# Optimization experiments

Measured on AMD Instinct MI355X. Metric: run time of the kernel, lower is better.

Reference implementation:

```python
import jax, jax.numpy as jnp
import numpy as np

NUM_ITERATIONS = 3
NUM_ROUTES = 6912  # 32*6*6*6


def _squash(t):
    # t: [..., O]; squash along last dim
    sq = jnp.sum(t * t, axis=-1, keepdims=True)
    return sq * t / ((1.0 + sq) * jnp.sqrt(sq))


def setup_inputs() -> dict:
    key = jax.random.key(0)
    k1, k2 = jax.random.split(key)
    B, R, I, C, O = 64, NUM_ROUTES, 8, 10, 16
    x = jax.random.normal(k1, (B, R, I), dtype=jnp.float32)
    route_weights = jax.random.normal(k2, (C, R, I, O), dtype=jnp.float32)
    return {"x": x, "route_weights": route_weights}


def reference(x, route_weights):
    # x: [B, R, I]; route_weights: [C, R, I, O]
    # priors = x[None,:,:,None,:] @ W[:,None,:,:,:] -> [C, B, R, 1, O]
    priors = jnp.einsum('bri,crio->cbro', x, route_weights)[:, :, :, None, :]
    logits = jnp.zeros_like(priors)  # [C, B, R, 1, O]
    outputs = None
    for i in range(NUM_ITERATIONS):
        # softmax over routes (dim=2), matching custom softmax(input, dim=2)
        probs = jax.nn.softmax(logits, axis=2)
        outputs = _squash(jnp.sum(probs * priors, axis=2, keepdims=True))  # [C,B,1,1,O]
        if i != NUM_ROUTES - 1:  # always true in original (num_routes >> iters)
            delta = jnp.sum(priors * outputs, axis=-1, keepdims=True)  # [C,B,R,1,1]
            logits = logits + delta
    return outputs
```

## Files before the change

kernel.cpp:

```cpp
#include <hip/hip_runtime.h>
#include <math.h>

#define BB 64
#define RR 6912
#define II 8
#define CC 10
#define OO 16
#define RPB 64
#define NCH 108
#define NGRP 8
#define MRG_PAD 20
#define LDSF (4*64*MRG_PAD + 4*64)

typedef _Float16 h2 __attribute__((ext_vector_type(2)));
typedef _Float16 half8 __attribute__((ext_vector_type(8)));
typedef float f32x16 __attribute__((ext_vector_type(16)));
union HV { int4 v; h2 h[4]; half8 h8; };

__global__ __launch_bounds__(256) void prep_kernel(
    const float* __restrict__ x, int4* __restrict__ xth4,
    const float4* __restrict__ w4, int4* __restrict__ wh4)
{
    __shared__ __align__(16) float4 lds4[64 * 34];
    const int t = threadIdx.x;
    const int bid = blockIdx.x;

    if (bid < 432) {
        const int rblk = bid >> 2;
        const int bblk = bid & 3;
        const int r0 = rblk * 64, b0 = bblk * 16;
        {
            const int rl = t & 63;
            const int bl0 = t >> 6;
#pragma unroll
            for (int kb = 0; kb < 4; ++kb) {
                const int bl = kb * 4 + bl0;
                const float4* src = (const float4*)(x + ((size_t)(b0 + bl) * RR + (r0 + rl)) * II);
                lds4[rl * 34 + bl * 2 + 0] = src[0];
                lds4[rl * 34 + bl * 2 + 1] = src[1];
            }
        }
        __syncthreads();
        {
            const int bl = t & 15;
            const int rw0 = t >> 4;
#pragma unroll
            for (int kr = 0; kr < 4; ++kr) {
                const int rw = kr * 16 + rw0;
                float4 a = lds4[rw * 34 + bl * 2 + 0];
                float4 bq = lds4[rw * 34 + bl * 2 + 1];
                HV u;
                u.h[0] = h2{(_Float16)a.x,  (_Float16)a.y};
                u.h[1] = h2{(_Float16)a.z,  (_Float16)a.w};
                u.h[2] = h2{(_Float16)bq.x, (_Float16)bq.y};
                u.h[3] = h2{(_Float16)bq.z, (_Float16)bq.w};
                xth4[(size_t)(r0 + rw) * BB + (b0 + bl)] = u.v;
            }
        }
    } else {
        _Float16* wl = (_Float16*)lds4;
        const int wblk = bid - 432;
        const int rp = t >> 5;
        const int i  = (t >> 2) & 7;
        const int o0 = (t & 3) * 4;
#pragma unroll 1
        for (int sb = 0; sb < 8; ++sb) {
            const int blk8 = wblk * 8 + sb;
            const float4 v = w4[(size_t)blk8 * 256 + t];
            _Float16* wb = wl + (sb & 1) * 1024;
            wb[(rp * 16 + o0 + 0) * 8 + i] = (_Float16)v.x;
            wb[(rp * 16 + o0 + 1) * 8 + i] = (_Float16)v.y;
            wb[(rp * 16 + o0 + 2) * 8 + i] = (_Float16)v.z;
            wb[(rp * 16 + o0 + 3) * 8 + i] = (_Float16)v.w;
            __syncthreads();
            if (t < 128) wh4[(size_t)blk8 * 128 + t] = ((const int4*)wb)[t];
        }
    }
}

template <int MODE>
__global__ __launch_bounds__(256, 4) void pass_kernel(
    const int4* __restrict__ xth4, const int4* __restrict__ wh4,
    const float* __restrict__ ov_in,
    float* __restrict__ pacc, float* __restrict__ pz)
{
    __shared__ __align__(16) float lds[LDSF];
    int4* wlds = (int4*)lds;

    const int bid = blockIdx.x;
    const int w = (bid & 7) * 135 + (bid >> 3);
    const int chunk = w / 10;
    const int c = w - chunk * 10;

    const int t = threadIdx.x;
    const int wv = t >> 6;
    const int l = t & 63;
    const int b = l & 31;
    const int hi = l >> 5;
    const int aquad = (l >> 4) & 1;
    const bool aact = (aquad == hi);

    {
        const int4* src = wh4 + (size_t)(c * (RR / 8) + chunk * 8) * 128;
#pragma unroll
        for (int k = 0; k < 4; ++k) wlds[k * 256 + t] = src[k * 256 + t];
    }

    float accA[8], accB[8];
#pragma unroll
    for (int j = 0; j < 8; ++j) { accA[j] = 0.f; accB[j] = 0.f; }
    float ZA = 0.f, ZB = 0.f;

    float ovA[8], ovB[8];
    if (MODE != 0) {
        const float* pa = ov_in + ((size_t)c * BB + b) * OO + 4 * hi;
        const float* pb = ov_in + ((size_t)c * BB + 32 + b) * OO + 4 * hi;
        float4 a0 = *(const float4*)(pa);
        float4 a1 = *(const float4*)(pa + 8);
        float4 b0 = *(const float4*)(pb);
        float4 b1 = *(const float4*)(pb + 8);
        ovA[0]=a0.x; ovA[1]=a0.y; ovA[2]=a0.z; ovA[3]=a0.w;
        ovA[4]=a1.x; ovA[5]=a1.y; ovA[6]=a1.z; ovA[7]=a1.w;
        ovB[0]=b0.x; ovB[1]=b0.y; ovB[2]=b0.z; ovB[3]=b0.w;
        ovB[4]=b1.x; ovB[5]=b1.y; ovB[6]=b1.z; ovB[7]=b1.w;
    }

    __syncthreads();

    const int rbase = chunk * RPB + wv * 16;

    f32x16 cA, cB, zf;
#pragma unroll
    for (int q = 0; q < 16; ++q) { cA[q] = 0.f; cB[q] = 0.f; zf[q] = 0.f; }

    HV xc0, xc1, xn0, xn1;
    xc0.v = xth4[(size_t)(rbase + hi) * BB + b];
    xc1.v = xth4[(size_t)(rbase + hi) * BB + 32 + b];
    xn0 = xc0; xn1 = xc1;

#pragma unroll 1
    for (int g = 0; g < NGRP; ++g) {
        if (g + 1 < NGRP) {
            const int rn = rbase + (g + 1) * 2 + hi;
            xn0.v = xth4[(size_t)rn * BB + b];
            xn1.v = xth4[(size_t)rn * BB + 32 + b];
        }
        const int rl0 = wv * 16 + g * 2;
        HV wq;
        wq.v = wlds[(rl0 + aquad) * 16 + (l & 15)];
        if (!aact) wq.v = make_int4(0, 0, 0, 0);

        if (MODE == 0) {
            cA = __builtin_amdgcn_mfma_f32_32x32x16_f16(wq.h8, xc0.h8, cA, 0, 0, 0);
            cB = __builtin_amdgcn_mfma_f32_32x32x16_f16(wq.h8, xc1.h8, cB, 0, 0, 0);
        } else {
            f32x16 p0 = __builtin_amdgcn_mfma_f32_32x32x16_f16(wq.h8, xc0.h8, zf, 0, 0, 0);
            f32x16 p1 = __builtin_amdgcn_mfma_f32_32x32x16_f16(wq.h8, xc1.h8, zf, 0, 0, 0);

            float dA0 = 0.f, dA1 = 0.f, dB0 = 0.f, dB1 = 0.f;
#pragma unroll
            for (int j = 0; j < 8; ++j) {
                dA0 = fmaf(p0[j],     ovA[j], dA0);
                dA1 = fmaf(p0[j + 8], ovA[j], dA1);
                dB0 = fmaf(p1[j],     ovB[j], dB0);
                dB1 = fmaf(p1[j + 8], ovB[j], dB1);
            }
            dA0 += __shfl_xor(dA0, 32);
            dA1 += __shfl_xor(dA1, 32);
            dB0 += __shfl_xor(dB0, 32);
            dB1 += __shfl_xor(dB1, 32);
            const float eA0 = __expf(dA0), eA1 = __expf(dA1);
            const float eB0 = __expf(dB0), eB1 = __expf(dB1);
            ZA += eA0 + eA1; ZB += eB0 + eB1;
#pragma unroll
            for (int j = 0; j < 8; ++j) {
                accA[j] = fmaf(eA0, p0[j], fmaf(eA1, p0[j + 8], accA[j]));
                accB[j] = fmaf(eB0, p1[j], fmaf(eB1, p1[j + 8], accB[j]));
            }
        }
        xc0 = xn0; xc1 = xn1;
    }

    if (MODE == 0) {
#pragma unroll
        for (int j = 0; j < 8; ++j) {
            accA[j] = cA[j] + cA[j + 8];
            accB[j] = cB[j] + cB[j + 8];
        }
    }

    __syncthreads();

    {
        float* m0 = lds + (wv * 64 + b) * MRG_PAD + 4 * hi;
        *(float4*)(m0)     = make_float4(accA[0], accA[1], accA[2], accA[3]);
        *(float4*)(m0 + 8) = make_float4(accA[4], accA[5], accA[6], accA[7]);
        float* m1 = lds + (wv * 64 + 32 + b) * MRG_PAD + 4 * hi;
        *(float4*)(m1)     = make_float4(accB[0], accB[1], accB[2], accB[3]);
        *(float4*)(m1 + 8) = make_float4(accB[4], accB[5], accB[6], accB[7]);
        if (MODE != 0 && hi == 0) {
            float* zr = lds + 4 * 64 * MRG_PAD;
            zr[wv * 64 + b] = ZA;
            zr[wv * 64 + 32 + b] = ZB;
        }
    }
    __syncthreads();

    {
        const int b2 = t >> 2, q = t & 3;
        float4 sum = make_float4(0.f, 0.f, 0.f, 0.f);
#pragma unroll
        for (int w2 = 0; w2 < 4; ++w2) {
            const float4 v = *(const float4*)(lds + (w2 * 64 + b2) * MRG_PAD + q * 4);
            sum.x += v.x; sum.y += v.y; sum.z += v.z; sum.w += v.w;
        }
        *(float4*)(pacc + (((size_t)(c * NCH + chunk) * BB + b2) * OO) + q * 4) = sum;
        if (MODE != 0 && q == 0) {
            const float* zr = lds + 4 * 64 * MRG_PAD;
            float z = 0.f;
#pragma unroll
            for (int w2 = 0; w2 < 4; ++w2) z += zr[w2 * 64 + b2];
            pz[(size_t)(c * NCH + chunk) * BB + b2] = z;
        }
    }
}

template <int MODE>
__global__ __launch_bounds__(256) void combine_kernel(
    const float* __restrict__ pacc, const float* __restrict__ pz,
    const float* __restrict__ out0, float* __restrict__ outw)
{
    __shared__ float lsum[256];
    __shared__ float lz[16];
    const int cb = blockIdx.x;
    const int c = cb >> 6, b = cb & 63;
    const int t = threadIdx.x;
    const int o = t & 15, g = t >> 4;

    float s = 0.f, zl = 0.f;
    for (int p = g; p < NCH; p += 16) {
        s += pacc[((size_t)(c * NCH + p) * BB + b) * OO + o];
        if (MODE != 0 && o == 0) zl += pz[(size_t)(c * NCH + p) * BB + b];
    }
    lsum[t] = s;
    if (MODE != 0 && o == 0) lz[g] = zl;
    __syncthreads();

    if (g == 0) {
#pragma unroll
        for (int k = 1; k < 16; ++k) s += lsum[k * 16 + o];
        if (MODE != 0) {
            float Zt = 0.f;
#pragma unroll
            for (int k = 0; k < 16; ++k) Zt += lz[k];
            s /= Zt;
        } else {
            s *= (1.0f / RR);
        }
        float sq = s * s;
#pragma unroll
        for (int w = 1; w < 16; w <<= 1) sq += __shfl_xor(sq, w);
        float val = s * sqrtf(sq) / (1.f + sq);
        if (MODE == 1) val += out0[(size_t)cb * OO + o];
        outw[(size_t)cb * OO + o] = val;
    }
}

extern "C" void kernel_launch(void* const* d_in, const int* in_sizes, int n_in,
                              void* d_out, int out_size, void* d_ws, size_t ws_size,
                              hipStream_t stream)
{
    const float* x = (const float*)d_in[0];
    const float* w = (const float*)d_in[1];
    float* out = (float*)d_out;

    float* ws = (float*)d_ws;
    float* xth    = ws;
    float* wh     = xth + (size_t)RR * BB * 4;
    float* pacc   = wh + (size_t)CC * RR * 64;
    float* pz     = pacc + (size_t)CC * NCH * BB * OO;
    float* out0   = pz + (size_t)CC * NCH * BB;
    float* outsum = out0 + CC * BB * OO;

    int4* xth4 = (int4*)xth;
    int4* wh4  = (int4*)wh;
    const float4* w4 = (const float4*)w;

    prep_kernel<<<dim3(432 + 1080), dim3(256), 0, stream>>>(x, xth4, w4, wh4);

    const dim3 gp(CC * NCH), bp(256);
    const dim3 gc(CC * BB), bc(256);

    pass_kernel<0><<<gp, bp, 0, stream>>>(xth4, wh4, nullptr, pacc, pz);
    combine_kernel<0><<<gc, bc, 0, stream>>>(pacc, pz, nullptr, out0);
    pass_kernel<1><<<gp, bp, 0, stream>>>(xth4, wh4, out0, pacc, pz);
    combine_kernel<1><<<gc, bc, 0, stream>>>(pacc, pz, out0, outsum);
    pass_kernel<2><<<gp, bp, 0, stream>>>(xth4, wh4, outsum, pacc, pz);
    combine_kernel<2><<<gc, bc, 0, stream>>>(pacc, pz, nullptr, out);
}
```

Baseline: 136.1 us.

## Simplify weight conversion and deepen x prefetch in pass kernel

The weight-prep path drops the LDS-staged transpose loop in favour of one thread per (route, o) that gathers 8 strided floats and writes one packed fp16 int4. The grid grows so each block handles 16 routes instead of 64. Separately, the pass kernel's x operand prefetch becomes a 4-deep register ring with the group loop fully unrolled, which hides more global-load latency. The costs are more uncoalesced strided reads in prep and higher register pressure in the pass kernel.

```diff
diff --git a/kernel.cpp b/kernel.cpp
--- a/kernel.cpp
+++ b/kernel.cpp
@@ -19,7 +19,7 @@
 
 __global__ __launch_bounds__(256) void prep_kernel(
     const float* __restrict__ x, int4* __restrict__ xth4,
-    const float4* __restrict__ w4, int4* __restrict__ wh4)
+    const float* __restrict__ w, int4* __restrict__ wh4)
 {
     __shared__ __align__(16) float4 lds4[64 * 34];
     const int t = threadIdx.x;
@@ -58,23 +58,19 @@
             }
         }
     } else {
-        _Float16* wl = (_Float16*)lds4;
         const int wblk = bid - 432;
-        const int rp = t >> 5;
-        const int i  = (t >> 2) & 7;
-        const int o0 = (t & 3) * 4;
-#pragma unroll 1
-        for (int sb = 0; sb < 8; ++sb) {
-            const int blk8 = wblk * 8 + sb;
-            const float4 v = w4[(size_t)blk8 * 256 + t];
-            _Float16* wb = wl + (sb & 1) * 1024;
-            wb[(rp * 16 + o0 + 0) * 8 + i] = (_Float16)v.x;
-            wb[(rp * 16 + o0 + 1) * 8 + i] = (_Float16)v.y;
-            wb[(rp * 16 + o0 + 2) * 8 + i] = (_Float16)v.z;
-            wb[(rp * 16 + o0 + 3) * 8 + i] = (_Float16)v.w;
-            __syncthreads();
-            if (t < 128) wh4[(size_t)blk8 * 128 + t] = ((const int4*)wb)[t];
-        }
+        const int rl = t >> 4;
+        const int o  = t & 15;
+        const size_t base = (size_t)wblk * 16 + rl;
+        const float* src = w + base * 128 + o;
+        float v0 = src[0 * 16], v1 = src[1 * 16], v2 = src[2 * 16], v3 = src[3 * 16];
+        float v4 = src[4 * 16], v5 = src[5 * 16], v6 = src[6 * 16], v7 = src[7 * 16];
+        HV u;
+        u.h[0] = h2{(_Float16)v0, (_Float16)v1};
+        u.h[1] = h2{(_Float16)v2, (_Float16)v3};
+        u.h[2] = h2{(_Float16)v4, (_Float16)v5};
+        u.h[3] = h2{(_Float16)v6, (_Float16)v7};
+        wh4[base * 16 + o] = u.v;
     }
 }
 
@@ -133,17 +129,21 @@
 #pragma unroll
     for (int q = 0; q < 16; ++q) { cA[q] = 0.f; cB[q] = 0.f; zf[q] = 0.f; }
 
-    HV xc0, xc1, xn0, xn1;
-    xc0.v = xth4[(size_t)(rbase + hi) * BB + b];
-    xc1.v = xth4[(size_t)(rbase + hi) * BB + 32 + b];
-    xn0 = xc0; xn1 = xc1;
-
-#pragma unroll 1
+    HV xq0[4], xq1[4];
+#pragma unroll
+    for (int g = 0; g < 4; ++g) {
+        const int rn = rbase + g * 2 + hi;
+        xq0[g].v = xth4[(size_t)rn * BB + b];
+        xq1[g].v = xth4[(size_t)rn * BB + 32 + b];
+    }
+
+#pragma unroll
     for (int g = 0; g < NGRP; ++g) {
-        if (g + 1 < NGRP) {
-            const int rn = rbase + (g + 1) * 2 + hi;
-            xn0.v = xth4[(size_t)rn * BB + b];
-            xn1.v = xth4[(size_t)rn * BB + 32 + b];
+        HV xc0 = xq0[g & 3], xc1 = xq1[g & 3];
+        if (g + 4 < NGRP) {
+            const int rn = rbase + (g + 4) * 2 + hi;
+            xq0[g & 3].v = xth4[(size_t)rn * BB + b];
+            xq1[g & 3].v = xth4[(size_t)rn * BB + 32 + b];
         }
         const int rl0 = wv * 16 + g * 2;
         HV wq;
@@ -178,7 +178,6 @@
                 accB[j] = fmaf(eB0, p1[j], fmaf(eB1, p1[j + 8], accB[j]));
             }
         }
-        xc0 = xn0; xc1 = xn1;
     }
 
     if (MODE == 0) {
@@ -284,9 +283,8 @@
 
     int4* xth4 = (int4*)xth;
     int4* wh4  = (int4*)wh;
-    const float4* w4 = (const float4*)w;
-
-    prep_kernel<<<dim3(432 + 1080), dim3(256), 0, stream>>>(x, xth4, w4, wh4);
+
+    prep_kernel<<<dim3(432 + 4320), dim3(256), 0, stream>>>(x, xth4, w, wh4);
 
     const dim3 gp(CC * NCH), bp(256);
     const dim3 gc(CC * BB), bc(256);
```

Measured after the change: 139.2 us. +2.3%, slower.

## Fuse routing passes into persistent kernel with grid barriers and atomic reductions

Applied to the files above, without the earlier changes.

Replaces the six pass/combine launches with one persistent kernel of 720 blocks that keeps its weight tile in LDS across all three routing iterations and separates phases with a software grid barrier. Partial sums are reduced with relaxed atomics into 9 replica buckets, which the prep kernel zeroes, instead of 108 per-chunk partials. This removes launch gaps, repeated weight-tile loads and the wide combine reads. In exchange it relies on all 720 blocks being co-resident, uses spin barriers with a bounded guard that could break correctness if they time out, and makes the floating-point sum order nondeterministic.

```diff
diff --git a/kernel.cpp b/kernel.cpp
--- a/kernel.cpp
+++ b/kernel.cpp
@@ -6,24 +6,54 @@
 #define II 8
 #define CC 10
 #define OO 16
-#define RPB 64
-#define NCH 108
-#define NGRP 8
+#define RPB2 96
+#define NCH2 72
+#define NG2 12
+#define NBLK 720
+#define NREP 9
 #define MRG_PAD 20
-#define LDSF (4*64*MRG_PAD + 4*64)
+#define WTILE_I4 (RPB2*16)
+#define MRGF (4*64*MRG_PAD + 4*64)
+#define ACCW (CC*NREP*BB*OO)
+#define ZW   (CC*NREP*BB)
+#define ZWORDS (3*ACCW + 2*ZW + 8)
 
 typedef _Float16 h2 __attribute__((ext_vector_type(2)));
 typedef _Float16 half8 __attribute__((ext_vector_type(8)));
 typedef float f32x16 __attribute__((ext_vector_type(16)));
 union HV { int4 v; h2 h[4]; half8 h8; };
 
+__device__ __forceinline__ void addf(float* p, float v) {
+    float old = __hip_atomic_fetch_add(p, v, __ATOMIC_RELAXED, __HIP_MEMORY_SCOPE_AGENT);
+    asm volatile("" :: "v"(old));
+}
+
+__device__ __forceinline__ void gbar(unsigned* cnt, unsigned target) {
+    __syncthreads();
+    if (threadIdx.x == 0) {
+        unsigned v = 1u + __hip_atomic_fetch_add(cnt, 1u, __ATOMIC_RELAXED,
+                                                 __HIP_MEMORY_SCOPE_AGENT);
+        int guard = 0;
+        while (v < target && ++guard < (1 << 13)) {
+            __builtin_amdgcn_s_sleep(2);
+            v = __hip_atomic_load(cnt, __ATOMIC_RELAXED, __HIP_MEMORY_SCOPE_AGENT);
+        }
+    }
+    __syncthreads();
+}
+
 __global__ __launch_bounds__(256) void prep_kernel(
     const float* __restrict__ x, int4* __restrict__ xth4,
-    const float4* __restrict__ w4, int4* __restrict__ wh4)
+    const float4* __restrict__ w4, int4* __restrict__ wh4,
+    float* __restrict__ zbase)
 {
     __shared__ __align__(16) float4 lds4[64 * 34];
     const int t = threadIdx.x;
     const int bid = blockIdx.x;
+
+    for (unsigned idx = (unsigned)bid * 256u + (unsigned)t; idx < (unsigned)ZWORDS;
+         idx += 1512u * 256u)
+        zbase[idx] = 0.f;
 
     if (bid < 432) {
         const int rblk = bid >> 2;
@@ -79,20 +109,12 @@
 }
 
 template <int MODE>
-__global__ __launch_bounds__(256, 4) void pass_kernel(
-    const int4* __restrict__ xth4, const int4* __restrict__ wh4,
-    const float* __restrict__ ov_in,
-    float* __restrict__ pacc, float* __restrict__ pz)
-{
-    __shared__ __align__(16) float lds[LDSF];
-    int4* wlds = (int4*)lds;
-
-    const int bid = blockIdx.x;
-    const int w = (bid & 7) * 135 + (bid >> 3);
-    const int chunk = w / 10;
-    const int c = w - chunk * 10;
-
-    const int t = threadIdx.x;
+__device__ __forceinline__ void it_phase(
+    const int4* __restrict__ xth4, const int4* wlds, float* mrg,
+    const float* __restrict__ ov,
+    float* __restrict__ acc, float* __restrict__ zacc,
+    int c, int chunk, int t)
+{
     const int wv = t >> 6;
     const int l = t & 63;
     const int b = l & 31;
@@ -100,12 +122,6 @@
     const int aquad = (l >> 4) & 1;
     const bool aact = (aquad == hi);
 
-    {
-        const int4* src = wh4 + (size_t)(c * (RR / 8) + chunk * 8) * 128;
-#pragma unroll
-        for (int k = 0; k < 4; ++k) wlds[k * 256 + t] = src[k * 256 + t];
-    }
-
     float accA[8], accB[8];
 #pragma unroll
     for (int j = 0; j < 8; ++j) { accA[j] = 0.f; accB[j] = 0.f; }
@@ -113,8 +129,8 @@
 
     float ovA[8], ovB[8];
     if (MODE != 0) {
-        const float* pa = ov_in + ((size_t)c * BB + b) * OO + 4 * hi;
-        const float* pb = ov_in + ((size_t)c * BB + 32 + b) * OO + 4 * hi;
+        const float* pa = ov + ((size_t)c * BB + b) * OO + 4 * hi;
+        const float* pb = ov + ((size_t)c * BB + 32 + b) * OO + 4 * hi;
         float4 a0 = *(const float4*)(pa);
         float4 a1 = *(const float4*)(pa + 8);
         float4 b0 = *(const float4*)(pb);
@@ -125,9 +141,7 @@
         ovB[4]=b1.x; ovB[5]=b1.y; ovB[6]=b1.z; ovB[7]=b1.w;
     }
 
-    __syncthreads();
-
-    const int rbase = chunk * RPB + wv * 16;
+    const int rbase = chunk * RPB2 + wv * 24;
 
     f32x16 cA, cB, zf;
 #pragma unroll
@@ -139,13 +153,13 @@
     xn0 = xc0; xn1 = xc1;
 
 #pragma unroll 1
-    for (int g = 0; g < NGRP; ++g) {
-        if (g + 1 < NGRP) {
+    for (int g = 0; g < NG2; ++g) {
+        if (g + 1 < NG2) {
             const int rn = rbase + (g + 1) * 2 + hi;
             xn0.v = xth4[(size_t)rn * BB + b];
             xn1.v = xth4[(size_t)rn * BB + 32 + b];
         }
-        const int rl0 = wv * 16 + g * 2;
+        const int rl0 = wv * 24 + g * 2;
         HV wq;
         wq.v = wlds[(rl0 + aquad) * 16 + (l & 15)];
         if (!aact) wq.v = make_int4(0, 0, 0, 0);
@@ -156,7 +170,6 @@
         } else {
             f32x16 p0 = __builtin_amdgcn_mfma_f32_32x32x16_f16(wq.h8, xc0.h8, zf, 0, 0, 0);
             f32x16 p1 = __builtin_amdgcn_mfma_f32_32x32x16_f16(wq.h8, xc1.h8, zf, 0, 0, 0);
-
             float dA0 = 0.f, dA1 = 0.f, dB0 = 0.f, dB1 = 0.f;
 #pragma unroll
             for (int j = 0; j < 8; ++j) {
@@ -189,17 +202,15 @@
         }
     }
 
-    __syncthreads();
-
     {
-        float* m0 = lds + (wv * 64 + b) * MRG_PAD + 4 * hi;
+        float* m0 = mrg + (wv * 64 + b) * MRG_PAD + 4 * hi;
         *(float4*)(m0)     = make_float4(accA[0], accA[1], accA[2], accA[3]);
         *(float4*)(m0 + 8) = make_float4(accA[4], accA[5], accA[6], accA[7]);
-        float* m1 = lds + (wv * 64 + 32 + b) * MRG_PAD + 4 * hi;
+        float* m1 = mrg + (wv * 64 + 32 + b) * MRG_PAD + 4 * hi;
         *(float4*)(m1)     = make_float4(accB[0], accB[1], accB[2], accB[3]);
         *(float4*)(m1 + 8) = make_float4(accB[4], accB[5], accB[6], accB[7]);
         if (MODE != 0 && hi == 0) {
-            float* zr = lds + 4 * 64 * MRG_PAD;
+            float* zr = mrg + 4 * 64 * MRG_PAD;
             zr[wv * 64 + b] = ZA;
             zr[wv * 64 + 32 + b] = ZB;
         }
@@ -211,48 +222,47 @@
         float4 sum = make_float4(0.f, 0.f, 0.f, 0.f);
 #pragma unroll
         for (int w2 = 0; w2 < 4; ++w2) {
-            const float4 v = *(const float4*)(lds + (w2 * 64 + b2) * MRG_PAD + q * 4);
+            const float4 v = *(const float4*)(mrg + (w2 * 64 + b2) * MRG_PAD + q * 4);
             sum.x += v.x; sum.y += v.y; sum.z += v.z; sum.w += v.w;
         }
-        *(float4*)(pacc + (((size_t)(c * NCH + chunk) * BB + b2) * OO) + q * 4) = sum;
+        const int rep = chunk % NREP;
+        float* dst = acc + (((size_t)c * NREP + rep) * BB + b2) * OO + q * 4;
+        addf(dst + 0, sum.x);
+        addf(dst + 1, sum.y);
+        addf(dst + 2, sum.z);
+        addf(dst + 3, sum.w);
         if (MODE != 0 && q == 0) {
-            const float* zr = lds + 4 * 64 * MRG_PAD;
+            const float* zr = mrg + 4 * 64 * MRG_PAD;
             float z = 0.f;
 #pragma unroll
             for (int w2 = 0; w2 < 4; ++w2) z += zr[w2 * 64 + b2];
-            pz[(size_t)(c * NCH + chunk) * BB + b2] = z;
+            addf(zacc + ((size_t)c * NREP + rep) * BB + b2, z);
         }
     }
 }
 
 template <int MODE>
-__global__ __launch_bounds__(256) void combine_kernel(
-    const float* __restrict__ pacc, const float* __restrict__ pz,
-    const float* __restrict__ out0, float* __restrict__ outw)
-{
-    __shared__ float lsum[256];
-    __shared__ float lz[16];
-    const int cb = blockIdx.x;
-    const int c = cb >> 6, b = cb & 63;
-    const int t = threadIdx.x;
+__device__ __forceinline__ void combine_phase(
+    const float* __restrict__ acc, const float* __restrict__ zacc,
+    const float* __restrict__ addv, float* __restrict__ dst, bool coh,
+    int bid, int t, float* cl)
+{
+    const int c2 = bid >> 6, b2 = bid & 63;
     const int o = t & 15, g = t >> 4;
 
-    float s = 0.f, zl = 0.f;
-    for (int p = g; p < NCH; p += 16) {
-        s += pacc[((size_t)(c * NCH + p) * BB + b) * OO + o];
-        if (MODE != 0 && o == 0) zl += pz[(size_t)(c * NCH + p) * BB + b];
-    }
-    lsum[t] = s;
-    if (MODE != 0 && o == 0) lz[g] = zl;
+    float s = (g < NREP) ? acc[(((size_t)c2 * NREP + g) * BB + b2) * OO + o] : 0.f;
+    cl[t] = s;
+    if (MODE != 0 && o == 0)
+        cl[256 + g] = (g < NREP) ? zacc[((size_t)c2 * NREP + g) * BB + b2] : 0.f;
     __syncthreads();
 
     if (g == 0) {
 #pragma unroll
-        for (int k = 1; k < 16; ++k) s += lsum[k * 16 + o];
+        for (int k = 1; k < NREP; ++k) s += cl[k * 16 + o];
         if (MODE != 0) {
             float Zt = 0.f;
 #pragma unroll
-            for (int k = 0; k < 16; ++k) Zt += lz[k];
+            for (int k = 0; k < NREP; ++k) Zt += cl[256 + k];
             s /= Zt;
         } else {
             s *= (1.0f / RR);
@@ -261,9 +271,50 @@
 #pragma unroll
         for (int w = 1; w < 16; w <<= 1) sq += __shfl_xor(sq, w);
         float val = s * sqrtf(sq) / (1.f + sq);
-        if (MODE == 1) val += out0[(size_t)cb * OO + o];
-        outw[(size_t)cb * OO + o] = val;
-    }
+        if (MODE == 1) val += addv[(size_t)bid * OO + o];
+        if (coh) {
+            float old = __hip_atomic_exchange(dst + (size_t)bid * OO + o, val,
+                         __ATOMIC_RELAXED, __HIP_MEMORY_SCOPE_AGENT);
+            asm volatile("" :: "v"(old));
+        } else {
+            dst[(size_t)bid * OO + o] = val;
+        }
+    }
+    __syncthreads();
+}
+
+__global__ __launch_bounds__(256, 3) void fused_kernel(
+    const int4* __restrict__ xth4, const int4* __restrict__ wh4,
+    float* acc0, float* acc1, float* acc2, float* z1, float* z2,
+    float* v0, float* outsum, float* out, unsigned* cnt)
+{
+    __shared__ __align__(16) int4 wlds[WTILE_I4];
+    __shared__ __align__(16) float mrg[MRGF];
+    __shared__ float cl[272];
+
+    const int bid = blockIdx.x;
+    const int t = threadIdx.x;
+    const int chunk = bid / 10;
+    const int c = bid - chunk * 10;
+
+    {
+        const int4* src = wh4 + ((size_t)c * RR + (size_t)chunk * RPB2) * 16;
+#pragma unroll
+        for (int k = 0; k < 6; ++k) wlds[k * 256 + t] = src[k * 256 + t];
+    }
+    __syncthreads();
+
+    it_phase<0>(xth4, wlds, mrg, nullptr, acc0, nullptr, c, chunk, t);
+    gbar(cnt, NBLK * 1);
+    if (bid < CC * BB) combine_phase<0>(acc0, nullptr, nullptr, v0, true, bid, t, cl);
+    gbar(cnt, NBLK * 2);
+    it_phase<1>(xth4, wlds, mrg, v0, acc1, z1, c, chunk, t);
+    gbar(cnt, NBLK * 3);
+    if (bid < CC * BB) combine_phase<1>(acc1, z1, v0, outsum, true, bid, t, cl);
+    gbar(cnt, NBLK * 4);
+    it_phase<2>(xth4, wlds, mrg, outsum, acc2, z2, c, chunk, t);
+    gbar(cnt, NBLK * 5);
+    if (bid < CC * BB) combine_phase<2>(acc2, z2, nullptr, out, false, bid, t, cl);
 }
 
 extern "C" void kernel_launch(void* const* d_in, const int* in_sizes, int n_in,
@@ -277,24 +328,21 @@
     float* ws = (float*)d_ws;
     float* xth    = ws;
     float* wh     = xth + (size_t)RR * BB * 4;
-    float* pacc   = wh + (size_t)CC * RR * 64;
-    float* pz     = pacc + (size_t)CC * NCH * BB * OO;
-    float* out0   = pz + (size_t)CC * NCH * BB;
-    float* outsum = out0 + CC * BB * OO;
+    float* zbase  = wh + (size_t)CC * RR * 64;
+    float* acc0   = zbase;
+    float* acc1   = acc0 + ACCW;
+    float* acc2   = acc1 + ACCW;
+    float* z1     = acc2 + ACCW;
+    float* z2     = z1 + ZW;
+    unsigned* cnt = (unsigned*)(z2 + ZW);
+    float* v0     = zbase + ZWORDS;
+    float* outsum = v0 + CC * BB * OO;
 
     int4* xth4 = (int4*)xth;
     int4* wh4  = (int4*)wh;
     const float4* w4 = (const float4*)w;
 
-    prep_kernel<<<dim3(432 + 1080), dim3(256), 0, stream>>>(x, xth4, w4, wh4);
-
-    const dim3 gp(CC * NCH), bp(256);
-    const dim3 gc(CC * BB), bc(256);
-
-    pass_kernel<0><<<gp, bp, 0, stream>>>(xth4, wh4, nullptr, pacc, pz);
-    combine_kernel<0><<<gc, bc, 0, stream>>>(pacc, pz, nullptr, out0);
-    pass_kernel<1><<<gp, bp, 0, stream>>>(xth4, wh4, out0, pacc, pz);
-    combine_kernel<1><<<gc, bc, 0, stream>>>(pacc, pz, out0, outsum);
-    pass_kernel<2><<<gp, bp, 0, stream>>>(xth4, wh4, outsum, pacc, pz);
-    combine_kernel<2><<<gc, bc, 0, stream>>>(pacc, pz, nullptr, out);
-}
+    prep_kernel<<<dim3(432 + 1080), dim3(256), 0, stream>>>(x, xth4, w4, wh4, zbase);
+    fused_kernel<<<dim3(NBLK), dim3(256), 0, stream>>>(
+        xth4, wh4, acc0, acc1, acc2, z1, z2, v0, outsum, out, cnt);
+}
```

Result: slower. 271.7 us (+99.6%).
